# Kernel tuning notes

Hardware: AMD Instinct MI355X
Metric: run time of the kernel (lower is better)

Reference implementation:

```python
import jax, jax.numpy as jnp
import numpy as np

TAIL_BOUND = 3.0
MIN_BIN_WIDTH = 1e-3
MIN_BIN_HEIGHT = 1e-3
SEARCH_EPS = 1e-6


def setup_inputs() -> dict:
    key = jax.random.key(0)
    k1, k2, k3, k4, k5 = jax.random.split(key, 5)
    B, D, K = 8192, 256, 8
    return {
        "x": jax.random.normal(k1, (B, D), dtype=jnp.float32),
        "w_": jax.random.normal(k2, (B, D, K), dtype=jnp.float32),
        "h_": jax.random.normal(k3, (B, D, K), dtype=jnp.float32),
        "dl_": jax.random.normal(k4, (B, D, 1), dtype=jnp.float32),
        "dr_": jax.random.normal(k5, (B, D, 1), dtype=jnp.float32),
    }


def _cumknots(unnorm, min_bin):
    # softmax -> min-width floor -> cumsum with exact 0/1 endpoints
    num_bins = unnorm.shape[-1]
    w = jax.nn.softmax(unnorm, axis=-1)
    w = min_bin + (1.0 - min_bin * num_bins) * w
    cum = jnp.cumsum(w, axis=-1)
    cum = cum.at[..., -1].set(1.0)
    pad = [(0, 0)] * (cum.ndim - 1) + [(1, 0)]
    cum = jnp.pad(cum, pad)
    return w, cum


def reference(x, w_, h_, dl_, dr_):
    num_bins = w_.shape[-1]
    left = bottom = -TAIL_BOUND
    right = top = TAIL_BOUND

    inside = (x >= left) & (x <= right)

    # map to unit interval; clamp keeps masked-out lanes numerically safe
    t = jnp.clip((x - left) / (right - left), 0.0, 1.0)

    widths, cumwidths = _cumknots(w_, MIN_BIN_WIDTH)       # [B,D,K], [B,D,K+1]
    heights, cumheights = _cumknots(h_, MIN_BIN_HEIGHT)

    slopes = heights / widths                              # [B,D,K]
    min1 = jnp.minimum(jnp.abs(slopes[..., :-1]), jnp.abs(slopes[..., 1:]))
    min2 = 0.5 * (widths[..., 1:] * slopes[..., :-1] + widths[..., :-1] * slopes[..., 1:]) \
           / (widths[..., :-1] + widths[..., 1:])
    mins = jnp.minimum(min1, min2)                         # [B,D,K-1]

    d_left = jax.nn.sigmoid(dl_) * 3.0 * slopes[..., :1]
    d_right = jax.nn.sigmoid(dr_) * 3.0 * slopes[..., -1:]
    d_mid = mins * (jnp.sign(slopes[..., :-1]) + jnp.sign(slopes[..., 1:]))
    derivs = jnp.concatenate([d_left, d_mid, d_right], axis=-1)  # [B,D,K+1]

    a = (derivs[..., :-1] + derivs[..., 1:] - 2.0 * slopes) / widths ** 2
    b = (3.0 * slopes - 2.0 * derivs[..., :-1] - derivs[..., 1:]) / widths
    c = derivs[..., :-1]
    d = cumheights[..., :-1]

    # searchsorted: sum(t >= knots) - 1, with eps bump on the last knot
    knots = cumwidths.at[..., -1].add(SEARCH_EPS)
    bin_idx = jnp.sum((t[..., None] >= knots).astype(jnp.int32), axis=-1) - 1
    bin_idx = jnp.clip(bin_idx, 0, num_bins - 1)[..., None]  # [B,D,1]

    take = lambda arr: jnp.take_along_axis(arr, bin_idx, axis=-1)[..., 0]
    ia, ib, ic, id_ = take(a), take(b), take(c), take(d)
    lw = take(cumwidths)

    sx = t - lw
    out_s = ia * sx ** 3 + ib * sx ** 2 + ic * sx + id_
    lad_s = jnp.log(jnp.abs(3.0 * ia * sx ** 2 + 2.0 * ib * sx + ic))

    out_s = jnp.clip(out_s, 0.0, 1.0) * (top - bottom) + bottom
    lad_s = lad_s + jnp.log(top - bottom) - jnp.log(right - left)

    outputs = jnp.where(inside, out_s, x)          # identity tails
    logabsdet = jnp.where(inside, lad_s, 0.0)
    return outputs, logabsdet
```

## Files before the change

kernel.cpp:

```cpp
#include <hip/hip_runtime.h>
#include <math.h>


constexpr int K = 8;
constexpr int E = 4;
constexpr float TAIL = 3.0f;
constexpr float MIN_BIN = 0.001f;

__device__ __forceinline__ float rcpf(float v) {
    return __builtin_amdgcn_rcpf(v);
}

__global__ __launch_bounds__(256, 4) void cbs_kernel(
    const float* __restrict__ x_,
    const float* __restrict__ w_,
    const float* __restrict__ h_,
    const float* __restrict__ dl_,
    const float* __restrict__ dr_,
    float* __restrict__ out,
    float* __restrict__ lad,
    int n)
{
    int tid  = blockIdx.x * blockDim.x + threadIdx.x;
    int base = tid * E;
    if (base >= n) return;

    float4 xv4 = *(const float4*)(x_  + base);
    float4 dl4 = *(const float4*)(dl_ + base);
    float4 dr4 = *(const float4*)(dr_ + base);
    const float4* w4 = (const float4*)w_ + 2 * (size_t)base;
    const float4* h4 = (const float4*)h_ + 2 * (size_t)base;

    float wv[E][K], hv[E][K];
    #pragma unroll
    for (int e = 0; e < E; e++) {
        float4 a = w4[2 * e], b = w4[2 * e + 1];
        wv[e][0] = a.x; wv[e][1] = a.y; wv[e][2] = a.z; wv[e][3] = a.w;
        wv[e][4] = b.x; wv[e][5] = b.y; wv[e][6] = b.z; wv[e][7] = b.w;
    }
    #pragma unroll
    for (int e = 0; e < E; e++) {
        float4 a = h4[2 * e], b = h4[2 * e + 1];
        hv[e][0] = a.x; hv[e][1] = a.y; hv[e][2] = a.z; hv[e][3] = a.w;
        hv[e][4] = b.x; hv[e][5] = b.y; hv[e][6] = b.z; hv[e][7] = b.w;
    }

    float xs[E]  = {xv4.x, xv4.y, xv4.z, xv4.w};
    float dls[E] = {dl4.x, dl4.y, dl4.z, dl4.w};
    float drs[E] = {dr4.x, dr4.y, dr4.z, dr4.w};
    float outs[E], lads[E];

    #pragma unroll
    for (int e = 0; e < E; e++) {
        float wr[K], hr[K];
        float sw = 0.0f, sh = 0.0f;
        #pragma unroll
        for (int k = 0; k < K; k++) { wr[k] = __expf(wv[e][k]); sw += wr[k]; }
        #pragma unroll
        for (int k = 0; k < K; k++) { hr[k] = __expf(hv[e][k]); sh += hr[k]; }
        float cwf = (1.0f - MIN_BIN * K) * rcpf(sw);
        float chf = (1.0f - MIN_BIN * K) * rcpf(sh);
        #pragma unroll
        for (int k = 0; k < K; k++) {
            wr[k] = fmaf(wr[k], cwf, MIN_BIN);
            hr[k] = fmaf(hr[k], chf, MIN_BIN);
        }

        float cw[K + 1], ch[K + 1], s[K];
        cw[0] = 0.0f; ch[0] = 0.0f;
        #pragma unroll
        for (int k = 0; k < K; k++) {
            cw[k + 1] = cw[k] + wr[k];
            ch[k + 1] = ch[k] + hr[k];
            s[k] = hr[k] * rcpf(wr[k]);
        }

        float dv[K + 1];
        dv[0] = 3.0f * s[0]     * rcpf(1.0f + __expf(-dls[e]));
        dv[K] = 3.0f * s[K - 1] * rcpf(1.0f + __expf(-drs[e]));
        #pragma unroll
        for (int k = 0; k < K - 1; k++) {
            float num = wr[k + 1] * s[k] + wr[k] * s[k + 1];
            dv[k + 1] = fminf(2.0f * fminf(s[k], s[k + 1]),
                              num * rcpf(wr[k] + wr[k + 1]));
        }

        float xv = xs[e];
        float t = fminf(fmaxf((xv + TAIL) * (1.0f / (2.0f * TAIL)), 0.0f), 1.0f);

        float wk = wr[0], sk = s[0], d0 = dv[0], d1 = dv[1], lw = 0.0f, dd = 0.0f;
        #pragma unroll
        for (int k = 1; k < K; k++) {
            bool p = (t >= cw[k]);
            wk = p ? wr[k]     : wk;
            sk = p ? s[k]      : sk;
            d0 = p ? dv[k]     : d0;
            d1 = p ? dv[k + 1] : d1;
            lw = p ? cw[k]     : lw;
            dd = p ? ch[k]     : dd;
        }

        float iw = rcpf(wk);
        float ia = (d0 + d1 - 2.0f * sk) * iw * iw;
        float ib = (3.0f * sk - 2.0f * d0 - d1) * iw;
        float sx = t - lw;
        float out_s = ((ia * sx + ib) * sx + d0) * sx + dd;
        float der   = (3.0f * ia * sx + 2.0f * ib) * sx + d0;
        float lad_s = __logf(fabsf(der));

        out_s = fminf(fmaxf(out_s, 0.0f), 1.0f) * (2.0f * TAIL) - TAIL;

        bool inside = (xv >= -TAIL) && (xv <= TAIL);
        outs[e] = inside ? out_s : xv;
        lads[e] = inside ? lad_s : 0.0f;
    }

    *(float4*)(out + base) = make_float4(outs[0], outs[1], outs[2], outs[3]);
    *(float4*)(lad + base) = make_float4(lads[0], lads[1], lads[2], lads[3]);
}

extern "C" void kernel_launch(void* const* d_in, const int* in_sizes, int n_in,
                              void* d_out, int out_size, void* d_ws, size_t ws_size,
                              hipStream_t stream) {
    const float* x  = (const float*)d_in[0];
    const float* w  = (const float*)d_in[1];
    const float* h  = (const float*)d_in[2];
    const float* dl = (const float*)d_in[3];
    const float* dr = (const float*)d_in[4];
    int n = in_sizes[0];
    float* out = (float*)d_out;
    float* lad = out + n;

    const int threads = 256;
    const int elems_per_block = threads * E;
    const int blocks = (n + elems_per_block - 1) / elems_per_block;
    cbs_kernel<<<blocks, threads, 0, stream>>>(x, w, h, dl, dr, out, lad, n);
}
```

Before: 179.0 us.

## Stage w/h through swizzled LDS for coalesced loads, one element per thread

Each thread now processes one element instead of four. Each wave loads its w and h rows with fully coalesced float4 reads into XOR-swizzled shared memory, then each lane reads back its own 8 values. The aim is to replace the strided per-thread 128-byte gathers with contiguous wave-wide accesses and to raise parallelism by launching four times more threads. The cost is extra LDS traffic, 16 KB of LDS per block, and scalar rather than vector loads and stores for x, dl, dr and the outputs.

```diff
diff --git a/kernel.cpp b/kernel.cpp
--- a/kernel.cpp
+++ b/kernel.cpp
@@ -3,7 +3,6 @@
 
 
 constexpr int K = 8;
-constexpr int E = 4;
 constexpr float TAIL = 3.0f;
 constexpr float MIN_BIN = 0.001f;
 
@@ -11,7 +10,11 @@
     return __builtin_amdgcn_rcpf(v);
 }
 
-__global__ __launch_bounds__(256, 4) void cbs_kernel(
+__device__ __forceinline__ unsigned swz(unsigned off) {
+    return off ^ ((off >> 3) & 0x70u);
+}
+
+__global__ __launch_bounds__(256) void cbs_kernel(
     const float* __restrict__ x_,
     const float* __restrict__ w_,
     const float* __restrict__ h_,
@@ -21,102 +24,101 @@
     float* __restrict__ lad,
     int n)
 {
-    int tid  = blockIdx.x * blockDim.x + threadIdx.x;
-    int base = tid * E;
-    if (base >= n) return;
+    __shared__ __align__(16) unsigned char lds[16384];
 
-    float4 xv4 = *(const float4*)(x_  + base);
-    float4 dl4 = *(const float4*)(dl_ + base);
-    float4 dr4 = *(const float4*)(dr_ + base);
-    const float4* w4 = (const float4*)w_ + 2 * (size_t)base;
-    const float4* h4 = (const float4*)h_ + 2 * (size_t)base;
+    int i = blockIdx.x * blockDim.x + threadIdx.x;
+    if (i >= n) return;
 
-    float wv[E][K], hv[E][K];
+    int wave = threadIdx.x >> 6;
+    int lane = threadIdx.x & 63;
+    size_t ebase = (size_t)blockIdx.x * 256 + (size_t)wave * 64;
+
+    const char* wg = (const char*)w_ + ebase * 32;
+    const char* hg = (const char*)h_ + ebase * 32;
+    unsigned wb = (unsigned)wave * 4096u;
+    unsigned hb = wb + 2048u;
+
     #pragma unroll
-    for (int e = 0; e < E; e++) {
-        float4 a = w4[2 * e], b = w4[2 * e + 1];
-        wv[e][0] = a.x; wv[e][1] = a.y; wv[e][2] = a.z; wv[e][3] = a.w;
-        wv[e][4] = b.x; wv[e][5] = b.y; wv[e][6] = b.z; wv[e][7] = b.w;
-    }
-    #pragma unroll
-    for (int e = 0; e < E; e++) {
-        float4 a = h4[2 * e], b = h4[2 * e + 1];
-        hv[e][0] = a.x; hv[e][1] = a.y; hv[e][2] = a.z; hv[e][3] = a.w;
-        hv[e][4] = b.x; hv[e][5] = b.y; hv[e][6] = b.z; hv[e][7] = b.w;
+    for (int r = 0; r < 2; r++) {
+        unsigned off = (unsigned)(r * 1024 + 16 * lane);
+        float4 vw = *(const float4*)(wg + off);
+        float4 vh = *(const float4*)(hg + off);
+        *(float4*)(&lds[wb + swz(off)]) = vw;
+        *(float4*)(&lds[hb + swz(off)]) = vh;
     }
 
-    float xs[E]  = {xv4.x, xv4.y, xv4.z, xv4.w};
-    float dls[E] = {dl4.x, dl4.y, dl4.z, dl4.w};
-    float drs[E] = {dr4.x, dr4.y, dr4.z, dr4.w};
-    float outs[E], lads[E];
+    float xv  = x_[i];
+    float dlv = dl_[i];
+    float drv = dr_[i];
 
+    unsigned o0 = 32u * (unsigned)lane;
+    float4 wa  = *(const float4*)(&lds[wb + swz(o0)]);
+    float4 wbv = *(const float4*)(&lds[wb + swz(o0 + 16u)]);
+    float4 ha  = *(const float4*)(&lds[hb + swz(o0)]);
+    float4 hbv = *(const float4*)(&lds[hb + swz(o0 + 16u)]);
+
+    float wr[K] = {wa.x, wa.y, wa.z, wa.w, wbv.x, wbv.y, wbv.z, wbv.w};
+    float hr[K] = {ha.x, ha.y, ha.z, ha.w, hbv.x, hbv.y, hbv.z, hbv.w};
+
+    float sw = 0.0f, sh = 0.0f;
     #pragma unroll
-    for (int e = 0; e < E; e++) {
-        float wr[K], hr[K];
-        float sw = 0.0f, sh = 0.0f;
-        #pragma unroll
-        for (int k = 0; k < K; k++) { wr[k] = __expf(wv[e][k]); sw += wr[k]; }
-        #pragma unroll
-        for (int k = 0; k < K; k++) { hr[k] = __expf(hv[e][k]); sh += hr[k]; }
-        float cwf = (1.0f - MIN_BIN * K) * rcpf(sw);
-        float chf = (1.0f - MIN_BIN * K) * rcpf(sh);
-        #pragma unroll
-        for (int k = 0; k < K; k++) {
-            wr[k] = fmaf(wr[k], cwf, MIN_BIN);
-            hr[k] = fmaf(hr[k], chf, MIN_BIN);
-        }
-
-        float cw[K + 1], ch[K + 1], s[K];
-        cw[0] = 0.0f; ch[0] = 0.0f;
-        #pragma unroll
-        for (int k = 0; k < K; k++) {
-            cw[k + 1] = cw[k] + wr[k];
-            ch[k + 1] = ch[k] + hr[k];
-            s[k] = hr[k] * rcpf(wr[k]);
-        }
-
-        float dv[K + 1];
-        dv[0] = 3.0f * s[0]     * rcpf(1.0f + __expf(-dls[e]));
-        dv[K] = 3.0f * s[K - 1] * rcpf(1.0f + __expf(-drs[e]));
-        #pragma unroll
-        for (int k = 0; k < K - 1; k++) {
-            float num = wr[k + 1] * s[k] + wr[k] * s[k + 1];
-            dv[k + 1] = fminf(2.0f * fminf(s[k], s[k + 1]),
-                              num * rcpf(wr[k] + wr[k + 1]));
-        }
-
-        float xv = xs[e];
-        float t = fminf(fmaxf((xv + TAIL) * (1.0f / (2.0f * TAIL)), 0.0f), 1.0f);
-
-        float wk = wr[0], sk = s[0], d0 = dv[0], d1 = dv[1], lw = 0.0f, dd = 0.0f;
-        #pragma unroll
-        for (int k = 1; k < K; k++) {
-            bool p = (t >= cw[k]);
-            wk = p ? wr[k]     : wk;
-            sk = p ? s[k]      : sk;
-            d0 = p ? dv[k]     : d0;
-            d1 = p ? dv[k + 1] : d1;
-            lw = p ? cw[k]     : lw;
-            dd = p ? ch[k]     : dd;
-        }
-
-        float iw = rcpf(wk);
-        float ia = (d0 + d1 - 2.0f * sk) * iw * iw;
-        float ib = (3.0f * sk - 2.0f * d0 - d1) * iw;
-        float sx = t - lw;
-        float out_s = ((ia * sx + ib) * sx + d0) * sx + dd;
-        float der   = (3.0f * ia * sx + 2.0f * ib) * sx + d0;
-        float lad_s = __logf(fabsf(der));
-
-        out_s = fminf(fmaxf(out_s, 0.0f), 1.0f) * (2.0f * TAIL) - TAIL;
-
-        bool inside = (xv >= -TAIL) && (xv <= TAIL);
-        outs[e] = inside ? out_s : xv;
-        lads[e] = inside ? lad_s : 0.0f;
+    for (int k = 0; k < K; k++) { wr[k] = __expf(wr[k]); sw += wr[k]; }
+    #pragma unroll
+    for (int k = 0; k < K; k++) { hr[k] = __expf(hr[k]); sh += hr[k]; }
+    float cwf = (1.0f - MIN_BIN * K) * rcpf(sw);
+    float chf = (1.0f - MIN_BIN * K) * rcpf(sh);
+    #pragma unroll
+    for (int k = 0; k < K; k++) {
+        wr[k] = fmaf(wr[k], cwf, MIN_BIN);
+        hr[k] = fmaf(hr[k], chf, MIN_BIN);
     }
 
-    *(float4*)(out + base) = make_float4(outs[0], outs[1], outs[2], outs[3]);
-    *(float4*)(lad + base) = make_float4(lads[0], lads[1], lads[2], lads[3]);
+    float cw[K + 1], ch[K + 1], s[K];
+    cw[0] = 0.0f; ch[0] = 0.0f;
+    #pragma unroll
+    for (int k = 0; k < K; k++) {
+        cw[k + 1] = cw[k] + wr[k];
+        ch[k + 1] = ch[k] + hr[k];
+        s[k] = hr[k] * rcpf(wr[k]);
+    }
+
+    float dv[K + 1];
+    dv[0] = 3.0f * s[0]     * rcpf(1.0f + __expf(-dlv));
+    dv[K] = 3.0f * s[K - 1] * rcpf(1.0f + __expf(-drv));
+    #pragma unroll
+    for (int k = 0; k < K - 1; k++) {
+        float num = wr[k + 1] * s[k] + wr[k] * s[k + 1];
+        dv[k + 1] = fminf(2.0f * fminf(s[k], s[k + 1]),
+                          num * rcpf(wr[k] + wr[k + 1]));
+    }
+
+    float t = fminf(fmaxf((xv + TAIL) * (1.0f / (2.0f * TAIL)), 0.0f), 1.0f);
+
+    float wk = wr[0], sk = s[0], d0 = dv[0], d1 = dv[1], lw = 0.0f, dd = 0.0f;
+    #pragma unroll
+    for (int k = 1; k < K; k++) {
+        bool p = (t >= cw[k]);
+        wk = p ? wr[k]     : wk;
+        sk = p ? s[k]      : sk;
+        d0 = p ? dv[k]     : d0;
+        d1 = p ? dv[k + 1] : d1;
+        lw = p ? cw[k]     : lw;
+        dd = p ? ch[k]     : dd;
+    }
+
+    float iw = rcpf(wk);
+    float ia = (d0 + d1 - 2.0f * sk) * iw * iw;
+    float ib = (3.0f * sk - 2.0f * d0 - d1) * iw;
+    float sx = t - lw;
+    float out_s = ((ia * sx + ib) * sx + d0) * sx + dd;
+    float der   = (3.0f * ia * sx + 2.0f * ib) * sx + d0;
+    float lad_s = __logf(fabsf(der));
+
+    out_s = fminf(fmaxf(out_s, 0.0f), 1.0f) * (2.0f * TAIL) - TAIL;
+
+    bool inside = (xv >= -TAIL) && (xv <= TAIL);
+    out[i] = inside ? out_s : xv;
+    lad[i] = inside ? lad_s : 0.0f;
 }
 
 extern "C" void kernel_launch(void* const* d_in, const int* in_sizes, int n_in,
@@ -132,7 +134,6 @@
     float* lad = out + n;
 
     const int threads = 256;
-    const int elems_per_block = threads * E;
-    const int blocks = (n + elems_per_block - 1) / elems_per_block;
+    const int blocks = (n + threads - 1) / threads;
     cbs_kernel<<<blocks, threads, 0, stream>>>(x, w, h, dl, dr, out, lad, n);
 }
```

New measurement: 175.6 us. Within noise of the previous version (-1.9%).
